# Kernel tuning notes

Measured on AMD Instinct MI355X. Metric: run time of the kernel, lower is better.

Reference implementation:

```python
import jax, jax.numpy as jnp
import numpy as np

B, T, D = 4, 2048, 512
H, DK = 4, 16
MU = 1.0


def _xavier(key, shape):
    lim = float(np.sqrt(6.0 / (shape[0] + shape[1])))
    return jax.random.uniform(key, shape, jnp.float32, -lim, lim)


def setup_inputs() -> dict:
    key = jax.random.key(0)
    ks = jax.random.split(key, 9)
    x = jax.random.normal(ks[0], (B, T, D), jnp.float32)
    Wq = _xavier(ks[1], (D, H * DK))
    Wk = _xavier(ks[2], (D, H * DK))
    Wv = _xavier(ks[3], (D, H * DK))
    # W_a is zero-initialized in the module; use small random values so the
    # decay path is exercised non-trivially.
    Wa = 0.02 * jax.random.normal(ks[4], (D, H), jnp.float32)
    ba = 0.02 * jax.random.normal(ks[5], (H,), jnp.float32)
    Wg = 0.02 * jax.random.normal(ks[6], (D, H * DK), jnp.float32)
    bg = jnp.zeros((H * DK,), jnp.float32)
    Wo = _xavier(ks[7], (H * DK, D))
    return {"x": x, "Wq": Wq, "Wk": Wk, "Wv": Wv, "Wa": Wa, "ba": ba,
            "Wg": Wg, "bg": bg, "Wo": Wo}


def reference(x, Wq, Wk, Wv, Wa, ba, Wg, bg, Wo):
    b_, t_, _ = x.shape
    q = (x @ Wq).reshape(b_, t_, H, DK)
    k = (x @ Wk).reshape(b_, t_, H, DK)
    v = (x @ Wv).reshape(b_, t_, H, DK)
    # bid b_s = <q_s, k_s>/sqrt(dk); decay a_s = -softplus(x W_a + c_a) <= 0
    bid = jnp.sum(q * k, axis=-1) / np.sqrt(DK)      # (B, T, H)
    a = -jax.nn.softplus(x @ Wa + ba)                # (B, T, H)
    # Closed form of the sequential scan:
    #   scores[t, s] = bid[s] + sum_{r=s+1..t} a[r] = (bid[s] - cumA[s]) + cumA[t]
    # Row-constant cumA[t] cancels in the softmax, so the attention weights are
    # a causal softmax over mu * (bid[s] - cumA[s]).
    cumA = jnp.cumsum(a, axis=1)                     # (B, T, H)
    lg = (bid - cumA).transpose(0, 2, 1)             # (B, H, S_keys)
    mask = jnp.tril(jnp.ones((t_, t_), bool))        # keys s <= query t
    scores = jnp.where(mask[None, None], MU * lg[:, :, None, :], -jnp.inf)
    w = jax.nn.softmax(scores, axis=-1)              # (B, H, T, S)
    y = jnp.einsum('bhts,bshd->bthd', w, v)          # (B, T, H, DK)
    gate = jax.nn.sigmoid(x @ Wg + bg).reshape(b_, t_, H, DK)
    y = (y * gate).reshape(b_, t_, H * DK)
    return y @ Wo
```

## Files before the change

### kernel.cpp

```cpp
#include <hip/hip_runtime.h>
#include <math.h>

#define B_    4
#define T_    2048
#define D_    512
#define H_    4
#define ROWS_ 8192
#define CHSZ_ 64
#define NCHK_ 32

typedef unsigned short ushort_t;
typedef unsigned int   uint_t;
typedef __attribute__((ext_vector_type(8))) __bf16         bfx8;
typedef __attribute__((ext_vector_type(8))) unsigned short u16x8;
typedef __attribute__((ext_vector_type(4))) float          fx4;

__device__ __forceinline__ ushort_t f2bf(float f) {
    union { float f; uint_t u; } v; v.f = f;
    return (ushort_t)((v.u + 0x7FFFu + ((v.u >> 16) & 1u)) >> 16);
}
__device__ __forceinline__ float bf2f(ushort_t u) {
    union { uint_t u; float f; } v; v.u = ((uint_t)u) << 16; return v.f;
}

__global__ __launch_bounds__(256) void pack_w(const float* __restrict__ Wq,
                                              const float* __restrict__ Wk,
                                              const float* __restrict__ Wv,
                                              const float* __restrict__ Wg,
                                              const float* __restrict__ Wo,
                                              ushort_t* __restrict__ WcatT2,
                                              ushort_t* __restrict__ WoT) {
    int idx = blockIdx.x * 256 + threadIdx.x;
    if (idx < 256 * 512) {
        int n = idx >> 9, d = idx & 511;
        int h = n >> 6, r = n & 63, part = r >> 4, j = r & 15;
        int col = h * 16 + j;
        const float* W = (part == 0) ? Wq : (part == 1) ? Wk : (part == 2) ? Wv : Wg;
        WcatT2[idx] = f2bf(W[(size_t)d * 64 + col]);
    } else {
        int r = idx - 256 * 512;
        int n = r >> 6, k = r & 63;
        WoT[r] = f2bf(Wo[(size_t)k * 512 + n]);
    }
}

__global__ __launch_bounds__(256) void gemm_scanA(const float* __restrict__ x,
                                                  const float* __restrict__ Wa,
                                                  const float* __restrict__ ba,
                                                  const ushort_t* __restrict__ WcatT2,
                                                  float* __restrict__ stateWS,
                                                  float* __restrict__ chunkSum,
                                                  ushort_t* __restrict__ gBuf) {
    __shared__ ushort_t As[64 * 72];
    __shared__ ushort_t Bs[64 * 72];
    __shared__ float s_wa[512];
    __shared__ float s_a[64];

    const int rc = blockIdx.x & 127;
    const int h  = blockIdx.x >> 7;
    const int m0 = rc * 64;
    const int n0 = h * 64;
    const int b  = rc >> 5, chunk = rc & 31;
    const int bh = b * 4 + h;

    const int tid = threadIdx.x;
    const int wave = tid >> 6, lane = tid & 63;
    const int fr = lane & 15, quad = lane >> 4;
    const int sr = tid >> 3, sc = (tid & 7) * 8;

    s_wa[tid * 2]     = Wa[(size_t)(tid * 2) * 4 + h];
    s_wa[tid * 2 + 1] = Wa[(size_t)(tid * 2 + 1) * 4 + h];

    fx4 acc[4];
    #pragma unroll
    for (int j = 0; j < 4; j++) acc[j] = (fx4)0.f;

    float pa[2] = {0.f, 0.f};

    float4 raF[2][2];
    u16x8  rb[2];
    #pragma unroll
    for (int s = 0; s < 2; s++) {
        const float* xp = x + (size_t)(m0 + s * 32 + sr) * D_ + sc;
        raF[s][0] = *(const float4*)xp;
        raF[s][1] = *(const float4*)(xp + 4);
        rb[s] = *(const u16x8*)(WcatT2 + (size_t)(n0 + s * 32 + sr) * D_ + sc);
    }

    __syncthreads();

    for (int it = 0; it < 8; it++) {
        const int kb = it * 64 + sc;
        #pragma unroll
        for (int s = 0; s < 2; s++) {
            float xv[8] = {raF[s][0].x, raF[s][0].y, raF[s][0].z, raF[s][0].w,
                           raF[s][1].x, raF[s][1].y, raF[s][1].z, raF[s][1].w};
            u16x8 u;
            #pragma unroll
            for (int j = 0; j < 8; j++) {
                u[j] = f2bf(xv[j]);
                pa[s] = fmaf(xv[j], s_wa[kb + j], pa[s]);
            }
            *(u16x8*)&As[(s * 32 + sr) * 72 + sc] = u;
            *(u16x8*)&Bs[(s * 32 + sr) * 72 + sc] = rb[s];
        }
        __syncthreads();
        if (it < 7) {
            const int k0 = (it + 1) * 64;
            #pragma unroll
            for (int s = 0; s < 2; s++) {
                const float* xp = x + (size_t)(m0 + s * 32 + sr) * D_ + k0 + sc;
                raF[s][0] = *(const float4*)xp;
                raF[s][1] = *(const float4*)(xp + 4);
                rb[s] = *(const u16x8*)(WcatT2 + (size_t)(n0 + s * 32 + sr) * D_ + k0 + sc);
            }
        }
        #pragma unroll
        for (int ks = 0; ks < 64; ks += 32) {
            bfx8 af = *(const bfx8*)&As[(wave * 16 + fr) * 72 + ks + quad * 8];
            #pragma unroll
            for (int ni = 0; ni < 4; ni++) {
                bfx8 bfr = *(const bfx8*)&Bs[(ni * 16 + fr) * 72 + ks + quad * 8];
                acc[ni] = __builtin_amdgcn_mfma_f32_16x16x32_bf16(af, bfr, acc[ni], 0, 0, 0);
            }
        }
        __syncthreads();
    }

    #pragma unroll
    for (int ni = 0; ni < 4; ni++)
        #pragma unroll
        for (int r = 0; r < 4; r++) {
            int rl = wave * 16 + quad * 4 + r;
            int cl = ni * 16 + fr;
            As[rl * 72 + cl] = f2bf(acc[ni][r]);
        }

    #pragma unroll
    for (int s = 0; s < 2; s++) {
        #pragma unroll
        for (int m = 1; m < 8; m <<= 1) pa[s] += __shfl_xor(pa[s], m, 8);
    }
    if ((tid & 7) == 0) {
        const float bah = ba[h];
        #pragma unroll
        for (int s = 0; s < 2; s++) {
            float z = pa[s] + bah;
            s_a[s * 32 + sr] = -(fmaxf(z, 0.f) + log1pf(expf(-fabsf(z))));
        }
    }
    __syncthreads();

    if (wave == 0) {
        const ushort_t* ct = &As[lane * 72];
        u16x8 q0 = *(const u16x8*)(ct +  0), q1 = *(const u16x8*)(ct +  8);
        u16x8 k0 = *(const u16x8*)(ct + 16), k1 = *(const u16x8*)(ct + 24);
        u16x8 v0 = *(const u16x8*)(ct + 32), v1 = *(const u16x8*)(ct + 40);
        float bid = 0.f;
        float v[16];
        #pragma unroll
        for (int j = 0; j < 8; j++) {
            bid = fmaf(bf2f(q0[j]), bf2f(k0[j]), bid);
            bid = fmaf(bf2f(q1[j]), bf2f(k1[j]), bid);
            v[j]     = bf2f(v0[j]);
            v[8 + j] = bf2f(v1[j]);
        }
        bid *= 0.25f;
        float a = s_a[lane];

        float ca = a;
        #pragma unroll
        for (int off = 1; off < 64; off <<= 1) {
            float up = __shfl_up(ca, off);
            if (lane >= off) ca += up;
        }

        float lg = bid - ca;

        float Mc = lg;
        #pragma unroll
        for (int off = 32; off; off >>= 1) Mc = fmaxf(Mc, __shfl_xor(Mc, off));

        float d = __expf(lg - Mc);
        float n[16];
        #pragma unroll
        for (int j = 0; j < 16; j++) n[j] = d * v[j];
        #pragma unroll
        for (int off = 1; off < 64; off <<= 1) {
            float ud = __shfl_up(d, off);
            float un[16];
            #pragma unroll
            for (int j = 0; j < 16; j++) un[j] = __shfl_up(n[j], off);
            if (lane >= off) {
                d += ud;
                #pragma unroll
                for (int j = 0; j < 16; j++) n[j] += un[j];
            }
        }

        const int t = chunk * CHSZ_ + lane;
        const size_t eidx = (size_t)bh * T_ + t;
        stateWS[eidx] = Mc;
        stateWS[32768 + eidx] = d;
        #pragma unroll
        for (int j = 0; j < 16; j++) stateWS[(size_t)(2 + j) * 32768 + eidx] = n[j];

        u16x8 g0 = *(const u16x8*)(ct + 48), g1 = *(const u16x8*)(ct + 56);
        *(u16x8*)(gBuf + eidx * 16)     = g0;
        *(u16x8*)(gBuf + eidx * 16 + 8) = g1;

        if (lane == 63) {
            float* cs = chunkSum + (size_t)(bh * NCHK_ + chunk) * 20;
            cs[0] = Mc; cs[1] = d;
            #pragma unroll
            for (int j = 0; j < 16; j++) cs[2 + j] = n[j];
            cs[18] = ca;
        }
    }
}

__global__ __launch_bounds__(256) void scan_gemm(const float* __restrict__ stateWS,
                                                 const float* __restrict__ chunkSum,
                                                 const ushort_t* __restrict__ gBuf,
                                                 const float* __restrict__ bg,
                                                 const ushort_t* __restrict__ WoT,
                                                 float* __restrict__ C) {
    __shared__ ushort_t Ys[64 * 72];
    __shared__ ushort_t Bs[128 * 72];
    __shared__ float s_pref[4][18];

    const int m0 = blockIdx.y * 64;
    const int n0 = blockIdx.x * 128;
    const int b  = m0 >> 11;
    const int tt = m0 & 2047;
    const int chunk = tt >> 6;

    const int tid = threadIdx.x;
    const int wave = tid >> 6, lane = tid & 63;

    const int sr = tid >> 3, sc = (tid & 7) * 8;
    #pragma unroll
    for (int s = 0; s < 4; s++) {
        int rr = s * 32 + sr;
        *(u16x8*)&Bs[rr * 72 + sc] = *(const u16x8*)(WoT + (size_t)(n0 + rr) * 64 + sc);
    }

    const int h = wave, r = lane;
    const int bh = b * 4 + h;
    const size_t eidx = (size_t)bh * T_ + tt + r;
    float m_row = stateWS[eidx];
    float d_row = stateWS[32768 + eidx];
    float n_row[16];
    #pragma unroll
    for (int j = 0; j < 16; j++) n_row[j] = stateWS[(size_t)(2 + j) * 32768 + eidx];
    u16x8 g0 = *(const u16x8*)(gBuf + eidx * 16);
    u16x8 g1 = *(const u16x8*)(gBuf + eidx * 16 + 8);

    if (wave < 2) {
        const int hh = wave * 2 + (lane >> 5), p = lane & 31;
        const int bhh = b * 4 + hh;
        float mf = -1e30f, dd = 0.f, aT = 0.f;
        float nn[16];
        #pragma unroll
        for (int j = 0; j < 16; j++) nn[j] = 0.f;
        if (p < chunk) {
            const float* cs = chunkSum + (size_t)(bhh * NCHK_ + p) * 20;
            mf = cs[0]; dd = cs[1];
            #pragma unroll
            for (int j = 0; j < 16; j++) nn[j] = cs[2 + j];
            aT = cs[18];
        }
        float off = aT;
        #pragma unroll
        for (int s = 1; s < 32; s <<= 1) {
            float t2 = __shfl_down(off, s, 32);
            if (p + s < chunk) off += t2;
        }
        if (p < chunk) mf += off;
        #pragma unroll
        for (int s = 1; s < 32; s <<= 1) {
            float m2 = __shfl_xor(mf, s, 32);
            float d2 = __shfl_xor(dd, s, 32);
            float mx = fmaxf(mf, m2);
            float al = __expf(mf - mx), be = __expf(m2 - mx);
            #pragma unroll
            for (int j = 0; j < 16; j++) {
                float n2 = __shfl_xor(nn[j], s, 32);
                nn[j] = nn[j] * al + n2 * be;
            }
            dd = dd * al + d2 * be;
            mf = mx;
        }
        if (p == 0) {
            s_pref[hh][0] = mf; s_pref[hh][1] = dd;
            #pragma unroll
            for (int j = 0; j < 16; j++) s_pref[hh][2 + j] = nn[j];
        }
    }
    __syncthreads();

    {
        const float M = s_pref[h][0], D = s_pref[h][1];
        const float mx = fmaxf(M, m_row);
        const float al = __expf(M - mx), be = __expf(m_row - mx);
        const float invd = 1.f / (D * al + d_row * be);
        u16x8 o0, o1;
        #pragma unroll
        for (int j = 0; j < 16; j++) {
            float Nj = s_pref[h][2 + j] * al + n_row[j] * be;
            float gpre = ((j < 8) ? bf2f(g0[j]) : bf2f(g1[j - 8])) + bg[h * 16 + j];
            float gate = 1.f / (1.f + __expf(-gpre));
            ushort_t yb = f2bf(Nj * invd * gate);
            if (j < 8) o0[j] = yb; else o1[j - 8] = yb;
        }
        *(u16x8*)&Ys[r * 72 + h * 16]     = o0;
        *(u16x8*)&Ys[r * 72 + h * 16 + 8] = o1;
    }
    __syncthreads();

    const int wr = wave >> 1, wc = wave & 1;
    const int fr = lane & 15, quad = lane >> 4;
    fx4 acc[2][4];
    #pragma unroll
    for (int i = 0; i < 2; i++)
        #pragma unroll
        for (int j = 0; j < 4; j++) acc[i][j] = (fx4)0.f;

    #pragma unroll
    for (int ks = 0; ks < 64; ks += 32) {
        bfx8 af[2], bfr[4];
        #pragma unroll
        for (int mi = 0; mi < 2; mi++)
            af[mi] = *(const bfx8*)&Ys[(wr * 32 + mi * 16 + fr) * 72 + ks + quad * 8];
        #pragma unroll
        for (int ni = 0; ni < 4; ni++)
            bfr[ni] = *(const bfx8*)&Bs[(wc * 64 + ni * 16 + fr) * 72 + ks + quad * 8];
        #pragma unroll
        for (int mi = 0; mi < 2; mi++)
            #pragma unroll
            for (int ni = 0; ni < 4; ni++)
                acc[mi][ni] = __builtin_amdgcn_mfma_f32_16x16x32_bf16(af[mi], bfr[ni], acc[mi][ni], 0, 0, 0);
    }

    #pragma unroll
    for (int mi = 0; mi < 2; mi++)
        #pragma unroll
        for (int ni = 0; ni < 4; ni++)
            #pragma unroll
            for (int rr = 0; rr < 4; rr++) {
                int orow = m0 + wr * 32 + mi * 16 + quad * 4 + rr;
                int ocol = n0 + wc * 64 + ni * 16 + fr;
                C[(size_t)orow * D_ + ocol] = acc[mi][ni][rr];
            }
}

extern "C" void kernel_launch(void* const* d_in, const int* in_sizes, int n_in,
                              void* d_out, int out_size, void* d_ws, size_t ws_size,
                              hipStream_t stream) {
    const float* x  = (const float*)d_in[0];
    const float* Wq = (const float*)d_in[1];
    const float* Wk = (const float*)d_in[2];
    const float* Wv = (const float*)d_in[3];
    const float* Wa = (const float*)d_in[4];
    const float* ba = (const float*)d_in[5];
    const float* Wg = (const float*)d_in[6];
    const float* bg = (const float*)d_in[7];
    const float* Wo = (const float*)d_in[8];
    float* out = (float*)d_out;

    char* w = (char*)d_ws;
    ushort_t* WcatT2   = (ushort_t*)w;  w += 256 * 512 * 2;
    ushort_t* WoT      = (ushort_t*)w;  w += 512 * 64 * 2;
    float*    stateWS  = (float*)w;     w += (size_t)18 * 32768 * 4;
    float*    chunkSum = (float*)w;     w += 512 * 20 * 4;
    ushort_t* gBuf     = (ushort_t*)w;  w += (size_t)32768 * 16 * 2;

    pack_w<<<640, 256, 0, stream>>>(Wq, Wk, Wv, Wg, Wo, WcatT2, WoT);
    gemm_scanA<<<512, 256, 0, stream>>>(x, Wa, ba, WcatT2,
                                        stateWS, chunkSum, gBuf);
    scan_gemm<<<dim3(4, 128), 256, 0, stream>>>(stateWS, chunkSum, gBuf, bg, WoT, out);
}
```

Measured before the change: 101.4 us.

## Double-buffer LDS tiles and prefetch two stages ahead in gemm_scanA

Splits the A and B shared-memory tiles into two ping-pong buffers, drops one of the two block barriers per k-iteration, and keeps two register stages of global prefetch in flight. The aim is to hide global-load latency and barrier stalls behind the MFMA work. It also switches to the compiler's native bf16 conversion and loads the Wa weights from shared memory as float4 instead of scalars. The cost is double the LDS footprint and more registers for the prefetch, which may reduce occupancy.

After: 102.5 us. No clear change (+1.1%).

```diff
diff --git a/kernel.cpp b/kernel.cpp
--- a/kernel.cpp
+++ b/kernel.cpp
@@ -18,6 +18,9 @@
 __device__ __forceinline__ ushort_t f2bf(float f) {
     union { float f; uint_t u; } v; v.f = f;
     return (ushort_t)((v.u + 0x7FFFu + ((v.u >> 16) & 1u)) >> 16);
+}
+__device__ __forceinline__ ushort_t f2bfc(float f) {
+    union { __bf16 h; ushort_t u; } v; v.h = (__bf16)f; return v.u;
 }
 __device__ __forceinline__ float bf2f(ushort_t u) {
     union { uint_t u; float f; } v; v.u = ((uint_t)u) << 16; return v.f;
@@ -51,8 +54,8 @@
                                                   float* __restrict__ stateWS,
                                                   float* __restrict__ chunkSum,
                                                   ushort_t* __restrict__ gBuf) {
-    __shared__ ushort_t As[64 * 72];
-    __shared__ ushort_t Bs[64 * 72];
+    __shared__ ushort_t As[2][64 * 72];
+    __shared__ ushort_t Bs[2][64 * 72];
     __shared__ float s_wa[512];
     __shared__ float s_a[64];
 
@@ -68,63 +71,78 @@
     const int fr = lane & 15, quad = lane >> 4;
     const int sr = tid >> 3, sc = (tid & 7) * 8;
 
+    fx4 acc[4];
+    #pragma unroll
+    for (int j = 0; j < 4; j++) acc[j] = (fx4)0.f;
+
+    float pa[2] = {0.f, 0.f};
+
+    float4 raF[2][2][2];
+    u16x8  rb[2][2];
+
+    #pragma unroll
+    for (int p = 0; p < 2; p++) {
+        const int k0 = p * 64;
+        #pragma unroll
+        for (int s = 0; s < 2; s++) {
+            const float* xp = x + (size_t)(m0 + s * 32 + sr) * D_ + k0 + sc;
+            raF[p][s][0] = *(const float4*)xp;
+            raF[p][s][1] = *(const float4*)(xp + 4);
+            rb[p][s] = *(const u16x8*)(WcatT2 + (size_t)(n0 + s * 32 + sr) * D_ + k0 + sc);
+        }
+    }
+
     s_wa[tid * 2]     = Wa[(size_t)(tid * 2) * 4 + h];
     s_wa[tid * 2 + 1] = Wa[(size_t)(tid * 2 + 1) * 4 + h];
 
-    fx4 acc[4];
-    #pragma unroll
-    for (int j = 0; j < 4; j++) acc[j] = (fx4)0.f;
-
-    float pa[2] = {0.f, 0.f};
-
-    float4 raF[2][2];
-    u16x8  rb[2];
-    #pragma unroll
-    for (int s = 0; s < 2; s++) {
-        const float* xp = x + (size_t)(m0 + s * 32 + sr) * D_ + sc;
-        raF[s][0] = *(const float4*)xp;
-        raF[s][1] = *(const float4*)(xp + 4);
-        rb[s] = *(const u16x8*)(WcatT2 + (size_t)(n0 + s * 32 + sr) * D_ + sc);
-    }
-
-    __syncthreads();
-
+    asm volatile("s_waitcnt lgkmcnt(0)" ::: "memory");
+    __builtin_amdgcn_sched_barrier(0);
+    __builtin_amdgcn_s_barrier();
+    __builtin_amdgcn_sched_barrier(0);
+
+    #pragma unroll
     for (int it = 0; it < 8; it++) {
+        const int cur = it & 1;
         const int kb = it * 64 + sc;
+        float4 wa0 = *(const float4*)&s_wa[kb];
+        float4 wa1 = *(const float4*)&s_wa[kb + 4];
+        float wav[8] = {wa0.x, wa0.y, wa0.z, wa0.w, wa1.x, wa1.y, wa1.z, wa1.w};
         #pragma unroll
         for (int s = 0; s < 2; s++) {
-            float xv[8] = {raF[s][0].x, raF[s][0].y, raF[s][0].z, raF[s][0].w,
-                           raF[s][1].x, raF[s][1].y, raF[s][1].z, raF[s][1].w};
+            float xv[8] = {raF[cur][s][0].x, raF[cur][s][0].y, raF[cur][s][0].z, raF[cur][s][0].w,
+                           raF[cur][s][1].x, raF[cur][s][1].y, raF[cur][s][1].z, raF[cur][s][1].w};
             u16x8 u;
             #pragma unroll
             for (int j = 0; j < 8; j++) {
-                u[j] = f2bf(xv[j]);
-                pa[s] = fmaf(xv[j], s_wa[kb + j], pa[s]);
-            }
-            *(u16x8*)&As[(s * 32 + sr) * 72 + sc] = u;
-            *(u16x8*)&Bs[(s * 32 + sr) * 72 + sc] = rb[s];
-        }
-        __syncthreads();
-        if (it < 7) {
-            const int k0 = (it + 1) * 64;
+                u[j] = f2bfc(xv[j]);
+                pa[s] = fmaf(xv[j], wav[j], pa[s]);
+            }
+            *(u16x8*)&As[cur][(s * 32 + sr) * 72 + sc] = u;
+            *(u16x8*)&Bs[cur][(s * 32 + sr) * 72 + sc] = rb[cur][s];
+        }
+        asm volatile("s_waitcnt lgkmcnt(0)" ::: "memory");
+        __builtin_amdgcn_sched_barrier(0);
+        __builtin_amdgcn_s_barrier();
+        __builtin_amdgcn_sched_barrier(0);
+        if (it < 6) {
+            const int k0 = (it + 2) * 64;
             #pragma unroll
             for (int s = 0; s < 2; s++) {
                 const float* xp = x + (size_t)(m0 + s * 32 + sr) * D_ + k0 + sc;
-                raF[s][0] = *(const float4*)xp;
-                raF[s][1] = *(const float4*)(xp + 4);
-                rb[s] = *(const u16x8*)(WcatT2 + (size_t)(n0 + s * 32 + sr) * D_ + k0 + sc);
+                raF[cur][s][0] = *(const float4*)xp;
+                raF[cur][s][1] = *(const float4*)(xp + 4);
+                rb[cur][s] = *(const u16x8*)(WcatT2 + (size_t)(n0 + s * 32 + sr) * D_ + k0 + sc);
             }
         }
         #pragma unroll
         for (int ks = 0; ks < 64; ks += 32) {
-            bfx8 af = *(const bfx8*)&As[(wave * 16 + fr) * 72 + ks + quad * 8];
+            bfx8 af = *(const bfx8*)&As[cur][(wave * 16 + fr) * 72 + ks + quad * 8];
             #pragma unroll
             for (int ni = 0; ni < 4; ni++) {
-                bfx8 bfr = *(const bfx8*)&Bs[(ni * 16 + fr) * 72 + ks + quad * 8];
+                bfx8 bfr = *(const bfx8*)&Bs[cur][(ni * 16 + fr) * 72 + ks + quad * 8];
                 acc[ni] = __builtin_amdgcn_mfma_f32_16x16x32_bf16(af, bfr, acc[ni], 0, 0, 0);
             }
         }
-        __syncthreads();
     }
 
     #pragma unroll
@@ -133,7 +151,7 @@
         for (int r = 0; r < 4; r++) {
             int rl = wave * 16 + quad * 4 + r;
             int cl = ni * 16 + fr;
-            As[rl * 72 + cl] = f2bf(acc[ni][r]);
+            As[0][rl * 72 + cl] = f2bfc(acc[ni][r]);
         }
 
     #pragma unroll
@@ -152,7 +170,7 @@
     __syncthreads();
 
     if (wave == 0) {
-        const ushort_t* ct = &As[lane * 72];
+        const ushort_t* ct = &As[0][lane * 72];
         u16x8 q0 = *(const u16x8*)(ct +  0), q1 = *(const u16x8*)(ct +  8);
         u16x8 k0 = *(const u16x8*)(ct + 16), k1 = *(const u16x8*)(ct + 24);
         u16x8 v0 = *(const u16x8*)(ct + 32), v1 = *(const u16x8*)(ct + 40);
```
